# Optimization experiments

Measured on AMD Instinct MI355X. Metric: run time of the kernel, lower is better.

## Reference

```python
import jax, jax.numpy as jnp
import numpy as np

B, H, L, D = 2, 8, 2048, 64

def setup_inputs() -> dict:
    key = jax.random.key(0)
    kq, kk, kv = jax.random.split(key, 3)
    q = jax.random.normal(kq, (B, H, L, D), dtype=jnp.float32)
    k = jax.random.normal(kk, (B, H, L, D), dtype=jnp.float32)
    v = jax.random.normal(kv, (B, H, L, D), dtype=jnp.float32)
    return {"q": q, "k": k, "v": v}

def reference(q, k, v):
    # attn = q @ k^T  -> [B, H, Lq, Lk]  (no softmax, no scaling, as in source)
    attn = jnp.einsum('bhqd,bhkd->bhqk', q, k)
    # output = attn @ v -> [B, H, Lq, D]
    out = jnp.einsum('bhqk,bhkd->bhqd', attn, v)
    return out
```

## Files before the change

kernel.cpp:

```cpp
#include <hip/hip_runtime.h>
#include <hip/hip_bf16.h>

#define BHN    16
#define LSEQ   2048
#define DDIM   64
#define CHUNK  128
#define NCHUNK (LSEQ / CHUNK)
#define NPART  (BHN * NCHUNK)

typedef unsigned short ushort8 __attribute__((ext_vector_type(8)));
typedef __bf16        bf16x8  __attribute__((ext_vector_type(8)));
typedef float         f32x4   __attribute__((ext_vector_type(4)));

__device__ __forceinline__ unsigned short f2bf(float f) {
    unsigned int u = __float_as_uint(f);
    u = u + 0x7FFFu + ((u >> 16) & 1u);
    return (unsigned short)(u >> 16);
}

__global__ __launch_bounds__(256) void k1_ktv(const float* __restrict__ Km,
                                              const float* __restrict__ Vm,
                                              float* __restrict__ P) {
    __shared__ float smem[16384];
    float* K_s = smem;
    float* V_s = smem + CHUNK * DDIM;

    const int pid   = blockIdx.x;
    const int bh    = pid >> 4;
    const int chunk = pid & 15;
    const int t     = threadIdx.x;

    const float* Kbase = Km + (size_t)bh * LSEQ * DDIM + (size_t)chunk * CHUNK * DDIM;
    const float* Vbase = Vm + (size_t)bh * LSEQ * DDIM + (size_t)chunk * CHUNK * DDIM;

    #pragma unroll
    for (int i = 0; i < 8; ++i) {
        int f4 = t + i * 256;
        ((float4*)K_s)[f4] = ((const float4*)Kbase)[f4];
        ((float4*)V_s)[f4] = ((const float4*)Vbase)[f4];
    }
    __syncthreads();

    const int w    = t >> 6;
    const int lane = t & 63;
    const int a    = lane & 7;
    const int b    = lane >> 3;

    float acc[8][8];
    #pragma unroll
    for (int i = 0; i < 8; ++i)
        #pragma unroll
        for (int j = 0; j < 8; ++j) acc[i][j] = 0.f;

    const float* Kw = K_s + (w * 32) * DDIM;
    const float* Vw = V_s + (w * 32) * DDIM;

    #pragma unroll 2
    for (int l = 0; l < 32; ++l) {
        float4 k0 = *(const float4*)(Kw + l * DDIM + a * 8);
        float4 k1 = *(const float4*)(Kw + l * DDIM + a * 8 + 4);
        float4 v0 = *(const float4*)(Vw + l * DDIM + b * 8);
        float4 v1 = *(const float4*)(Vw + l * DDIM + b * 8 + 4);
        float kk[8] = {k0.x, k0.y, k0.z, k0.w, k1.x, k1.y, k1.z, k1.w};
        float vv[8] = {v0.x, v0.y, v0.z, v0.w, v1.x, v1.y, v1.z, v1.w};
        #pragma unroll
        for (int j2 = 0; j2 < 8; ++j2)
            #pragma unroll
            for (int j1 = 0; j1 < 8; ++j1)
                acc[j2][j1] = fmaf(kk[j1], vv[j2], acc[j2][j1]);
    }
    __syncthreads();

    float* R = smem;
    #pragma unroll
    for (int j2 = 0; j2 < 8; ++j2) {
        int row = b * 8 + j2;
        int pc  = (a ^ j2) * 8;
        float* dst = R + w * 4096 + row * 64 + pc;
        *(float4*)(dst)     = float4{acc[j2][0], acc[j2][1], acc[j2][2], acc[j2][3]};
        *(float4*)(dst + 4) = float4{acc[j2][4], acc[j2][5], acc[j2][6], acc[j2][7]};
    }
    __syncthreads();

    float* Pout = P + (size_t)pid * 4096;
    #pragma unroll
    for (int i = 0; i < 16; ++i) {
        int e   = t + i * 256;
        int row = e >> 6;
        int col = e & 63;
        int pcc = col ^ ((row & 7) << 3);
        int idx = row * 64 + pcc;
        float s = R[idx] + R[4096 + idx] + R[8192 + idx] + R[12288 + idx];
        Pout[e] = s;
    }
}

__global__ __launch_bounds__(256) void k2_reduce(const float* __restrict__ P,
                                                 unsigned short* __restrict__ MT) {
    const int blk = blockIdx.x;
    const int bh  = blk >> 4;
    const int seg = blk & 15;
    const int e   = seg * 256 + threadIdx.x;
    float s = 0.f;
    #pragma unroll
    for (int c = 0; c < 16; ++c)
        s += P[(size_t)(bh * 16 + c) * 4096 + e];
    MT[(size_t)bh * 4096 + e] = f2bf(s);
}

__global__ __launch_bounds__(256) void k3_qm(const float* __restrict__ Q,
                                             const unsigned short* __restrict__ MT,
                                             float* __restrict__ Out) {
    const int pid  = blockIdx.x;
    const int bh   = pid >> 5;
    const int rb   = pid & 31;
    const int t    = threadIdx.x;
    const int w    = t >> 6;
    const int lane = t & 63;
    const int q0   = rb * 64 + w * 16;
    const int r    = lane & 15;
    const int g    = lane >> 4;

    const float* Qb = Q + (size_t)bh * LSEQ * DDIM;

    union Frag { ushort8 u; bf16x8 b; };
    Frag afrag[2];
    #pragma unroll
    for (int s = 0; s < 2; ++s) {
        const float* qp = Qb + (size_t)(q0 + r) * DDIM + s * 32 + g * 8;
        float4 x0 = *(const float4*)qp;
        float4 x1 = *(const float4*)(qp + 4);
        afrag[s].u = (ushort8){f2bf(x0.x), f2bf(x0.y), f2bf(x0.z), f2bf(x0.w),
                               f2bf(x1.x), f2bf(x1.y), f2bf(x1.z), f2bf(x1.w)};
    }

    const unsigned short* Mb = MT + (size_t)bh * 4096;
    f32x4 acc[4];
    #pragma unroll
    for (int nt = 0; nt < 4; ++nt) {
        acc[nt] = (f32x4){0.f, 0.f, 0.f, 0.f};
        #pragma unroll
        for (int s = 0; s < 2; ++s) {
            Frag bfrag;
            bfrag.u = *(const ushort8*)(Mb + (nt * 16 + r) * 64 + s * 32 + g * 8);
            acc[nt] = __builtin_amdgcn_mfma_f32_16x16x32_bf16(afrag[s].b, bfrag.b,
                                                              acc[nt], 0, 0, 0);
        }
    }

    float* Ob = Out + (size_t)bh * LSEQ * DDIM;
    #pragma unroll
    for (int nt = 0; nt < 4; ++nt)
        #pragma unroll
        for (int j = 0; j < 4; ++j)
            Ob[(size_t)(q0 + g * 4 + j) * DDIM + nt * 16 + r] = acc[nt][j];
}

extern "C" void kernel_launch(void* const* d_in, const int* in_sizes, int n_in,
                              void* d_out, int out_size, void* d_ws, size_t ws_size,
                              hipStream_t stream) {
    const float* q = (const float*)d_in[0];
    const float* k = (const float*)d_in[1];
    const float* v = (const float*)d_in[2];
    float* out = (float*)d_out;

    float*          P  = (float*)d_ws;
    unsigned short* MT = (unsigned short*)((char*)d_ws +
                          (size_t)NPART * 4096 * sizeof(float));

    k1_ktv   <<<NPART, 256, 0, stream>>>(k, v, P);
    k2_reduce<<<256,   256, 0, stream>>>(P, MT);
    k3_qm    <<<BHN * 32, 256, 0, stream>>>(q, MT, out);
}
```

Before: 85.17 us.

## Fuse three attention kernels into one cooperative kernel with grid syncs

Merges the K^T·V partial product, the chunk reduction and the Q·M MFMA stage into a single cooperative launch, separated by grid-wide barriers. The goal is to remove two kernel launch gaps. In exchange, the reduction now runs on only 16 blocks with 16 elements per thread, which leaves most of the grid idle during that phase. The final stage covers 128 rows per block and reuses the M fragments held in registers. Grid syncs add their own cost, and all 256 blocks must be co-resident for the cooperative launch to succeed.

After: 213.4 us. 151% more time.

```diff
diff --git a/kernel.cpp b/kernel.cpp
--- a/kernel.cpp
+++ b/kernel.cpp
@@ -1,5 +1,8 @@
 #include <hip/hip_runtime.h>
 #include <hip/hip_bf16.h>
+#include <hip/hip_cooperative_groups.h>
+
+namespace cg = cooperative_groups;
 
 #define BHN    16
 #define LSEQ   2048
@@ -18,142 +21,154 @@
     return (unsigned short)(u >> 16);
 }
 
-__global__ __launch_bounds__(256) void k1_ktv(const float* __restrict__ Km,
-                                              const float* __restrict__ Vm,
-                                              float* __restrict__ P) {
+union Frag { ushort8 u; bf16x8 b; };
+
+__global__ __launch_bounds__(256)
+void fused_attn(const float* __restrict__ Q,
+                const float* __restrict__ Km,
+                const float* __restrict__ Vm,
+                float* __restrict__ Out,
+                float* __restrict__ P,
+                unsigned short* __restrict__ MT) {
     __shared__ float smem[16384];
-    float* K_s = smem;
-    float* V_s = smem + CHUNK * DDIM;
+    const int pid = blockIdx.x;
+    const int t   = threadIdx.x;
 
-    const int pid   = blockIdx.x;
-    const int bh    = pid >> 4;
-    const int chunk = pid & 15;
-    const int t     = threadIdx.x;
+    {
+        float* K_s = smem;
+        float* V_s = smem + CHUNK * DDIM;
+        const int bh    = pid >> 4;
+        const int chunk = pid & 15;
 
-    const float* Kbase = Km + (size_t)bh * LSEQ * DDIM + (size_t)chunk * CHUNK * DDIM;
-    const float* Vbase = Vm + (size_t)bh * LSEQ * DDIM + (size_t)chunk * CHUNK * DDIM;
+        const float* Kbase = Km + (size_t)bh * LSEQ * DDIM + (size_t)chunk * CHUNK * DDIM;
+        const float* Vbase = Vm + (size_t)bh * LSEQ * DDIM + (size_t)chunk * CHUNK * DDIM;
 
-    #pragma unroll
-    for (int i = 0; i < 8; ++i) {
-        int f4 = t + i * 256;
-        ((float4*)K_s)[f4] = ((const float4*)Kbase)[f4];
-        ((float4*)V_s)[f4] = ((const float4*)Vbase)[f4];
-    }
-    __syncthreads();
+        #pragma unroll
+        for (int i = 0; i < 8; ++i) {
+            int f4 = t + i * 256;
+            ((float4*)K_s)[f4] = ((const float4*)Kbase)[f4];
+            ((float4*)V_s)[f4] = ((const float4*)Vbase)[f4];
+        }
+        __syncthreads();
 
-    const int w    = t >> 6;
-    const int lane = t & 63;
-    const int a    = lane & 7;
-    const int b    = lane >> 3;
+        const int w    = t >> 6;
+        const int lane = t & 63;
+        const int a    = lane & 7;
+        const int b    = lane >> 3;
 
-    float acc[8][8];
-    #pragma unroll
-    for (int i = 0; i < 8; ++i)
+        float acc[8][8];
         #pragma unroll
-        for (int j = 0; j < 8; ++j) acc[i][j] = 0.f;
+        for (int i = 0; i < 8; ++i)
+            #pragma unroll
+            for (int j = 0; j < 8; ++j) acc[i][j] = 0.f;
 
-    const float* Kw = K_s + (w * 32) * DDIM;
-    const float* Vw = V_s + (w * 32) * DDIM;
+        const float* Kw = K_s + (w * 32) * DDIM;
+        const float* Vw = V_s + (w * 32) * DDIM;
 
-    #pragma unroll 2
-    for (int l = 0; l < 32; ++l) {
-        float4 k0 = *(const float4*)(Kw + l * DDIM + a * 8);
-        float4 k1 = *(const float4*)(Kw + l * DDIM + a * 8 + 4);
-        float4 v0 = *(const float4*)(Vw + l * DDIM + b * 8);
-        float4 v1 = *(const float4*)(Vw + l * DDIM + b * 8 + 4);
-        float kk[8] = {k0.x, k0.y, k0.z, k0.w, k1.x, k1.y, k1.z, k1.w};
-        float vv[8] = {v0.x, v0.y, v0.z, v0.w, v1.x, v1.y, v1.z, v1.w};
+        #pragma unroll 2
+        for (int l = 0; l < 32; ++l) {
+            float4 k0 = *(const float4*)(Kw + l * DDIM + a * 8);
+            float4 k1 = *(const float4*)(Kw + l * DDIM + a * 8 + 4);
+            float4 v0 = *(const float4*)(Vw + l * DDIM + b * 8);
+            float4 v1 = *(const float4*)(Vw + l * DDIM + b * 8 + 4);
+            float kk[8] = {k0.x, k0.y, k0.z, k0.w, k1.x, k1.y, k1.z, k1.w};
+            float vv[8] = {v0.x, v0.y, v0.z, v0.w, v1.x, v1.y, v1.z, v1.w};
+            #pragma unroll
+            for (int j2 = 0; j2 < 8; ++j2)
+                #pragma unroll
+                for (int j1 = 0; j1 < 8; ++j1)
+                    acc[j2][j1] = fmaf(kk[j1], vv[j2], acc[j2][j1]);
+        }
+        __syncthreads();
+
+        float* R = smem;
         #pragma unroll
-        for (int j2 = 0; j2 < 8; ++j2)
-            #pragma unroll
-            for (int j1 = 0; j1 < 8; ++j1)
-                acc[j2][j1] = fmaf(kk[j1], vv[j2], acc[j2][j1]);
-    }
-    __syncthreads();
+        for (int j2 = 0; j2 < 8; ++j2) {
+            int row = b * 8 + j2;
+            int pc  = (a ^ j2) * 8;
+            float* dst = R + w * 4096 + row * 64 + pc;
+            *(float4*)(dst)     = float4{acc[j2][0], acc[j2][1], acc[j2][2], acc[j2][3]};
+            *(float4*)(dst + 4) = float4{acc[j2][4], acc[j2][5], acc[j2][6], acc[j2][7]};
+        }
+        __syncthreads();
 
-    float* R = smem;
-    #pragma unroll
-    for (int j2 = 0; j2 < 8; ++j2) {
-        int row = b * 8 + j2;
-        int pc  = (a ^ j2) * 8;
-        float* dst = R + w * 4096 + row * 64 + pc;
-        *(float4*)(dst)     = float4{acc[j2][0], acc[j2][1], acc[j2][2], acc[j2][3]};
-        *(float4*)(dst + 4) = float4{acc[j2][4], acc[j2][5], acc[j2][6], acc[j2][7]};
-    }
-    __syncthreads();
-
-    float* Pout = P + (size_t)pid * 4096;
-    #pragma unroll
-    for (int i = 0; i < 16; ++i) {
-        int e   = t + i * 256;
-        int row = e >> 6;
-        int col = e & 63;
-        int pcc = col ^ ((row & 7) << 3);
-        int idx = row * 64 + pcc;
-        float s = R[idx] + R[4096 + idx] + R[8192 + idx] + R[12288 + idx];
-        Pout[e] = s;
-    }
-}
-
-__global__ __launch_bounds__(256) void k2_reduce(const float* __restrict__ P,
-                                                 unsigned short* __restrict__ MT) {
-    const int blk = blockIdx.x;
-    const int bh  = blk >> 4;
-    const int seg = blk & 15;
-    const int e   = seg * 256 + threadIdx.x;
-    float s = 0.f;
-    #pragma unroll
-    for (int c = 0; c < 16; ++c)
-        s += P[(size_t)(bh * 16 + c) * 4096 + e];
-    MT[(size_t)bh * 4096 + e] = f2bf(s);
-}
-
-__global__ __launch_bounds__(256) void k3_qm(const float* __restrict__ Q,
-                                             const unsigned short* __restrict__ MT,
-                                             float* __restrict__ Out) {
-    const int pid  = blockIdx.x;
-    const int bh   = pid >> 5;
-    const int rb   = pid & 31;
-    const int t    = threadIdx.x;
-    const int w    = t >> 6;
-    const int lane = t & 63;
-    const int q0   = rb * 64 + w * 16;
-    const int r    = lane & 15;
-    const int g    = lane >> 4;
-
-    const float* Qb = Q + (size_t)bh * LSEQ * DDIM;
-
-    union Frag { ushort8 u; bf16x8 b; };
-    Frag afrag[2];
-    #pragma unroll
-    for (int s = 0; s < 2; ++s) {
-        const float* qp = Qb + (size_t)(q0 + r) * DDIM + s * 32 + g * 8;
-        float4 x0 = *(const float4*)qp;
-        float4 x1 = *(const float4*)(qp + 4);
-        afrag[s].u = (ushort8){f2bf(x0.x), f2bf(x0.y), f2bf(x0.z), f2bf(x0.w),
-                               f2bf(x1.x), f2bf(x1.y), f2bf(x1.z), f2bf(x1.w)};
-    }
-
-    const unsigned short* Mb = MT + (size_t)bh * 4096;
-    f32x4 acc[4];
-    #pragma unroll
-    for (int nt = 0; nt < 4; ++nt) {
-        acc[nt] = (f32x4){0.f, 0.f, 0.f, 0.f};
+        float* Pout = P + (size_t)pid * 4096;
         #pragma unroll
-        for (int s = 0; s < 2; ++s) {
-            Frag bfrag;
-            bfrag.u = *(const ushort8*)(Mb + (nt * 16 + r) * 64 + s * 32 + g * 8);
-            acc[nt] = __builtin_amdgcn_mfma_f32_16x16x32_bf16(afrag[s].b, bfrag.b,
-                                                              acc[nt], 0, 0, 0);
+        for (int i = 0; i < 16; ++i) {
+            int e   = t + i * 256;
+            int row = e >> 6;
+            int col = e & 63;
+            int pcc = col ^ ((row & 7) << 3);
+            int idx = row * 64 + pcc;
+            Pout[e] = R[idx] + R[4096 + idx] + R[8192 + idx] + R[12288 + idx];
         }
     }
 
-    float* Ob = Out + (size_t)bh * LSEQ * DDIM;
-    #pragma unroll
-    for (int nt = 0; nt < 4; ++nt)
+    __threadfence();
+    cg::this_grid().sync();
+
+    if (pid < BHN) {
+        const int bh = pid;
         #pragma unroll
-        for (int j = 0; j < 4; ++j)
-            Ob[(size_t)(q0 + g * 4 + j) * DDIM + nt * 16 + r] = acc[nt][j];
+        for (int i = 0; i < 16; ++i) {
+            int e = t + i * 256;
+            float s = 0.f;
+            #pragma unroll
+            for (int c = 0; c < 16; ++c)
+                s += P[(size_t)(bh * 16 + c) * 4096 + e];
+            MT[(size_t)bh * 4096 + e] = f2bf(s);
+        }
+    }
+
+    __threadfence();
+    cg::this_grid().sync();
+
+    {
+        const int w    = t >> 6;
+        const int lane = t & 63;
+        const int r    = lane & 15;
+        const int g    = lane >> 4;
+        const int bh   = pid >> 4;
+        const int rb2  = pid & 15;
+
+        const float*          Qb = Q   + (size_t)bh * LSEQ * DDIM;
+        float*                Ob = Out + (size_t)bh * LSEQ * DDIM;
+        const unsigned short* Mb = MT  + (size_t)bh * 4096;
+
+        Frag bfrag[4][2];
+        #pragma unroll
+        for (int nt = 0; nt < 4; ++nt)
+            #pragma unroll
+            for (int s = 0; s < 2; ++s)
+                bfrag[nt][s].u = *(const ushort8*)(Mb + (nt * 16 + r) * 64 + s * 32 + g * 8);
+
+        #pragma unroll
+        for (int rr = 0; rr < 2; ++rr) {
+            const int q0 = rb2 * 128 + rr * 64 + w * 16;
+
+            Frag afrag[2];
+            #pragma unroll
+            for (int s = 0; s < 2; ++s) {
+                const float* qp = Qb + (size_t)(q0 + r) * DDIM + s * 32 + g * 8;
+                float4 x0 = *(const float4*)qp;
+                float4 x1 = *(const float4*)(qp + 4);
+                afrag[s].u = (ushort8){f2bf(x0.x), f2bf(x0.y), f2bf(x0.z), f2bf(x0.w),
+                                       f2bf(x1.x), f2bf(x1.y), f2bf(x1.z), f2bf(x1.w)};
+            }
+
+            #pragma unroll
+            for (int nt = 0; nt < 4; ++nt) {
+                f32x4 acc = (f32x4){0.f, 0.f, 0.f, 0.f};
+                #pragma unroll
+                for (int s = 0; s < 2; ++s)
+                    acc = __builtin_amdgcn_mfma_f32_16x16x32_bf16(afrag[s].b, bfrag[nt][s].b,
+                                                                  acc, 0, 0, 0);
+                #pragma unroll
+                for (int j = 0; j < 4; ++j)
+                    Ob[(size_t)(q0 + g * 4 + j) * DDIM + nt * 16 + r] = acc[j];
+            }
+        }
+    }
 }
 
 extern "C" void kernel_launch(void* const* d_in, const int* in_sizes, int n_in,
@@ -168,7 +183,7 @@
     unsigned short* MT = (unsigned short*)((char*)d_ws +
                           (size_t)NPART * 4096 * sizeof(float));
 
-    k1_ktv   <<<NPART, 256, 0, stream>>>(k, v, P);
-    k2_reduce<<<256,   256, 0, stream>>>(P, MT);
-    k3_qm    <<<BHN * 32, 256, 0, stream>>>(q, MT, out);
+    void* args[] = {(void*)&q, (void*)&k, (void*)&v, (void*)&out, (void*)&P, (void*)&MT};
+    hipLaunchCooperativeKernel((void*)fused_attn, dim3(NPART), dim3(256),
+                               args, 0, stream);
 }
```
